# Kernel optimization log

Hardware: AMD Instinct MI355X
Metric: run time of the kernel (lower is better)

The kernel has to match this reference:

```python
import jax, jax.numpy as jnp
import numpy as np

B, C, H, W = 2, 224, 56, 56
NUM_HEADS, HEAD_DIM = 7, 32  # C == NUM_HEADS * HEAD_DIM
EPS = 1e-5


def setup_inputs() -> dict:
    key = jax.random.key(0)
    ks = jax.random.split(key, 16)
    n = lambda k, shape, s=0.05: jax.random.normal(k, shape, dtype=jnp.float32) * s
    return {
        "D": n(ks[0], (B, C, H, W), 1.0),
        "wq": n(ks[1], (2 * C, C)), "bq": n(ks[2], (2 * C,)),
        "wk": n(ks[3], (2 * C, C)), "bk": n(ks[4], (2 * C,)),
        "wv": n(ks[5], (C, C)), "bv": n(ks[6], (C,)),
        "gn_w": jnp.ones((C,), jnp.float32), "gn_b": jnp.zeros((C,), jnp.float32),
        "lambda_init": jnp.array(0.4, jnp.float32),
        "lq1": n(ks[7], (HEAD_DIM,), 0.1), "lk1": n(ks[8], (HEAD_DIM,), 0.1),
        "lq2": n(ks[9], (HEAD_DIM,), 0.1), "lk2": n(ks[10], (HEAD_DIM,), 0.1),
        "w3": n(ks[11], (C, C, 3, 3), 0.02), "b3": n(ks[12], (C,)),
        "wo": n(ks[13], (1, C)), "bo": n(ks[14], (1,)),
    }


def _conv1x1(x, w, b):
    # 1x1 conv == channel-mixing matmul: w [O,C], x [B,C,H,W] -> [B,O,H,W]
    return jnp.einsum('oc,bchw->bohw', w, x) + b[None, :, None, None]


def reference(D, wq, bq, wk, bk, wv, bv, gn_w, gn_b, lambda_init,
              lq1, lk1, lq2, lk2, w3, b3, wo, bo):
    b, c, h_, w_ = D.shape
    N = h_ * w_
    scaling = HEAD_DIM ** (-0.5)

    # spatial coordinate gating: pool over W and over H, broadcast-sum
    x_h = D.mean(axis=3, keepdims=True)          # [B,C,H,1]
    x_w = D.mean(axis=2, keepdims=True)          # [B,C,1,W]
    gated = D * jax.nn.sigmoid(x_h + x_w)

    # GroupNorm with num_groups == C  => per-channel instance norm (biased var)
    mu = gated.mean(axis=(2, 3), keepdims=True)
    var = gated.var(axis=(2, 3), keepdims=True)
    spatial_enh = (gated - mu) / jnp.sqrt(var + EPS)
    spatial_enh = spatial_enh * gn_w[None, :, None, None] + gn_b[None, :, None, None]

    Q = _conv1x1(spatial_enh, wq, bq).reshape(b, 2, NUM_HEADS, HEAD_DIM, N)
    K = _conv1x1(D, wk, bk).reshape(b, 2, NUM_HEADS, HEAD_DIM, N)
    V = _conv1x1(D, wv, bv).reshape(b, NUM_HEADS, HEAD_DIM, N)

    attn1 = jnp.einsum('bhdn,bhdm->bhnm', Q[:, 0], K[:, 0]) * scaling
    attn2 = jnp.einsum('bhdn,bhdm->bhnm', Q[:, 1], K[:, 1]) * scaling

    lam1 = jnp.exp(jnp.sum(lq1 * lk1))
    lam2 = jnp.exp(jnp.sum(lq2 * lk2))
    lam = jnp.clip(lam1 - lam2, 0.0, 1.0) + lambda_init

    attn_weights = jax.nn.softmax(attn1 - lam * attn2, axis=-1)
    out = jnp.einsum('bhnm,bhdm->bhdn', attn_weights, V).reshape(b, c, h_, w_)

    x1 = jax.nn.sigmoid(out.mean(axis=(2, 3), keepdims=True))  # [B,C,1,1]
    x2 = jax.lax.conv_general_dilated(
        out, w3, window_strides=(1, 1), padding='SAME',
        dimension_numbers=('NCHW', 'OIHW', 'NCHW')) + b3[None, :, None, None]
    cross_enh = x2 * x1
    attn_map = jax.nn.sigmoid(_conv1x1(cross_enh, wo, bo))  # [B,1,H,W]
    return attn_map
```

## Files before the change

### kernel.cpp

```cpp
#include <hip/hip_runtime.h>
#include <math.h>

#define NPIX 3136
#define CCH  224
#define SCALING 0.17677669529663687f
#define LOG2E 1.4426950408889634f
#define SCL2 (SCALING * LOG2E)

typedef _Float16 half8_t __attribute__((ext_vector_type(8)));
typedef _Float16 half4_t __attribute__((ext_vector_type(4)));
typedef _Float16 half2_t __attribute__((ext_vector_type(2)));
typedef float floatx4 __attribute__((ext_vector_type(4)));

__device__ __forceinline__ float exp2fast(float x) { return __builtin_amdgcn_exp2f(x); }

__device__ __forceinline__ void blockReduce2(float& a, float& b, float* scratch) {
  #pragma unroll
  for (int off = 32; off > 0; off >>= 1) {
    a += __shfl_down(a, off);
    b += __shfl_down(b, off);
  }
  int wid = threadIdx.x >> 6, lane = threadIdx.x & 63;
  if (lane == 0) { scratch[wid * 2] = a; scratch[wid * 2 + 1] = b; }
  __syncthreads();
  if (threadIdx.x == 0) {
    float sa = 0.f, sb = 0.f;
    #pragma unroll
    for (int i = 0; i < 4; ++i) { sa += scratch[2 * i]; sb += scratch[2 * i + 1]; }
    scratch[0] = sa; scratch[1] = sb;
  }
  __syncthreads();
  a = scratch[0]; b = scratch[1];
}

__global__ void lam_kernel(const float* __restrict__ lq1, const float* __restrict__ lk1,
                           const float* __restrict__ lq2, const float* __restrict__ lk2,
                           const float* __restrict__ lambda_init, float* __restrict__ lam) {
  int t = threadIdx.x;
  float p1 = (t < 32) ? lq1[t] * lk1[t] : 0.f;
  float p2 = (t < 32) ? lq2[t] * lk2[t] : 0.f;
  #pragma unroll
  for (int off = 16; off > 0; off >>= 1) {
    p1 += __shfl_down(p1, off);
    p2 += __shfl_down(p2, off);
  }
  if (t == 0) {
    float d = expf(p1) - expf(p2);
    d = fminf(fmaxf(d, 0.f), 1.f);
    lam[0] = d + lambda_init[0];
  }
}

__global__ __launch_bounds__(256) void prep_kernel(const float* __restrict__ D,
                                                   const float* __restrict__ gn_w,
                                                   const float* __restrict__ gn_b,
                                                   _Float16* __restrict__ senh_h,
                                                   _Float16* __restrict__ Dh) {
  __shared__ float img[NPIX];
  __shared__ float xh[56];
  __shared__ float xw[56];
  __shared__ float scratch[8];
  int bc = blockIdx.x;
  int c = bc % CCH;
  const float* src = D + (size_t)bc * NPIX;
  float4* img4 = (float4*)img;
  const float4* src4 = (const float4*)src;
  half4_t* dh4 = (half4_t*)(Dh + (size_t)bc * NPIX);
  for (int i = threadIdx.x; i < NPIX / 4; i += 256) {
    float4 v = src4[i];
    img4[i] = v;
    half4_t hv;
    hv[0] = (_Float16)v.x; hv[1] = (_Float16)v.y;
    hv[2] = (_Float16)v.z; hv[3] = (_Float16)v.w;
    dh4[i] = hv;
  }
  __syncthreads();
  if (threadIdx.x < 56) {
    int h = threadIdx.x;
    float s = 0.f;
    #pragma unroll 8
    for (int w = 0; w < 56; ++w) s += img[h * 56 + w];
    xh[h] = s * (1.f / 56.f);
  } else if (threadIdx.x >= 64 && threadIdx.x < 120) {
    int w = threadIdx.x - 64;
    float s = 0.f;
    #pragma unroll 8
    for (int h = 0; h < 56; ++h) s += img[h * 56 + w];
    xw[w] = s * (1.f / 56.f);
  }
  __syncthreads();
  float sum = 0.f, ssq = 0.f;
  for (int i = threadIdx.x; i < NPIX; i += 256) {
    int y = i / 56, x = i - y * 56;
    float d = img[i];
    float t = xh[y] + xw[x];
    float sg = 1.f / (1.f + __expf(-t));
    float g = d * sg;
    img[i] = g;
    sum += g;
    ssq += g * g;
  }
  blockReduce2(sum, ssq, scratch);
  float mu = sum * (1.f / (float)NPIX);
  float var = ssq * (1.f / (float)NPIX) - mu * mu;
  float rstd = rsqrtf(var + 1e-5f);
  float a = gn_w[c] * rstd;
  float bb = gn_b[c] - mu * a;
  _Float16* dst = senh_h + (size_t)bc * NPIX;
  for (int i = threadIdx.x; i < NPIX; i += 256) dst[i] = (_Float16)fmaf(img[i], a, bb);
}

__global__ void wcvt_kernel(const float* __restrict__ wq, const float* __restrict__ wk,
                            const float* __restrict__ wv,
                            _Float16* __restrict__ whq, _Float16* __restrict__ whk,
                            _Float16* __restrict__ whv) {
  int i = blockIdx.x * 256 + threadIdx.x;
  const int NQ = 448 * 224 / 4;
  const int NV = 224 * 224 / 4;
  const float* src; _Float16* dst; int off;
  if (i < NQ) { src = wq; dst = whq; off = i; }
  else if (i < 2 * NQ) { src = wk; dst = whk; off = i - NQ; }
  else if (i < 2 * NQ + NV) { src = wv; dst = whv; off = i - 2 * NQ; }
  else return;
  float4 v = ((const float4*)src)[off];
  half4_t h;
  h[0] = (_Float16)v.x; h[1] = (_Float16)v.y;
  h[2] = (_Float16)v.z; h[3] = (_Float16)v.w;
  ((half4_t*)dst)[off] = h;
}

__global__ __launch_bounds__(256) void gemm_f16_kernel(const _Float16* __restrict__ Wh,
                                                       const _Float16* __restrict__ Xh,
                                                       const float* __restrict__ bias,
                                                       _Float16* __restrict__ Y, int M, int mode,
                                                       const float* __restrict__ lamp) {
  __shared__ _Float16 Xs[64][40];
  __shared__ _Float16 Cs[64][72];
  int b = blockIdx.z;
  int r0 = blockIdx.y * 64, n0 = blockIdx.x * 64;
  const _Float16* Xb = Xh + (size_t)b * CCH * NPIX;
  int tid = threadIdx.x;
  int w = tid >> 6, lane = tid & 63, q = lane & 15, g = lane >> 4;

  int wrow = r0 + w * 16 + q;
  if (wrow >= M) wrow = M - 1;
  half8_t wfrag[7];
  #pragma unroll
  for (int kc = 0; kc < 7; ++kc)
    wfrag[kc] = *(const half8_t*)&Wh[(size_t)wrow * 224 + kc * 32 + g * 8];

  floatx4 acc[4];
  #pragma unroll
  for (int t = 0; t < 4; ++t)
    #pragma unroll
    for (int r = 0; r < 4; ++r) acc[t][r] = 0.f;

  int cp = tid & 15, ng = tid >> 4;
  #pragma unroll
  for (int kc = 0; kc < 7; ++kc) {
    const _Float16* x0 = Xb + (size_t)(kc * 32 + 2 * cp) * NPIX + n0 + ng * 4;
    half4_t xa = *(const half4_t*)x0;
    half4_t xb = *(const half4_t*)(x0 + NPIX);
    if (kc) __syncthreads();
    #pragma unroll
    for (int j = 0; j < 4; ++j) {
      half2_t hw; hw[0] = xa[j]; hw[1] = xb[j];
      *(half2_t*)&Xs[ng * 4 + j][2 * cp] = hw;
    }
    __syncthreads();
    #pragma unroll
    for (int t = 0; t < 4; ++t) {
      half8_t xfrag = *(const half8_t*)&Xs[16 * t + q][g * 8];
      acc[t] = __builtin_amdgcn_mfma_f32_16x16x32_f16(wfrag[kc], xfrag, acc[t], 0, 0, 0);
    }
  }

  float lamv = (mode == 1) ? lamp[0] : 0.f;
  #pragma unroll
  for (int t = 0; t < 4; ++t) {
    #pragma unroll
    for (int r = 0; r < 4; ++r) {
      int m = w * 16 + 4 * g + r;
      int n = 16 * t + q;
      int gm = r0 + m;
      float v = 0.f;
      if (gm < M) {
        v = acc[t][r] + bias[gm];
        if (mode == 1) v *= (gm < CCH) ? SCL2 : (-lamv * SCL2);
      }
      Cs[m][n] = (_Float16)v;
    }
  }
  __syncthreads();

  if (mode == 0) {
    int row = tid >> 2, oct = tid & 3;
    if (r0 + row < M) {
      half8_t u0 = *(half8_t*)&Cs[row][oct * 16];
      half8_t u1 = *(half8_t*)&Cs[row][oct * 16 + 8];
      _Float16* dst = Y + ((size_t)b * M + r0 + row) * NPIX + n0 + oct * 16;
      *(half8_t*)dst = u0;
      *(half8_t*)(dst + 8) = u1;
    }
  } else {
    int n = tid & 63, quarter = tid >> 6;
    int vbase = r0 + quarter * 16;
    int chunk = vbase >= CCH;
    int ch_in = vbase - chunk * CCH;
    int hh = ch_in >> 5;
    int dstart = chunk * 32 + (ch_in & 31);
    _Float16 tmp[16];
    #pragma unroll
    for (int i = 0; i < 16; ++i) tmp[i] = Cs[quarter * 16 + i][n];
    _Float16* dst = Y + (((size_t)b * 7 + hh) * NPIX + (n0 + n)) * 64 + dstart;
    *(half8_t*)dst = *(half8_t*)&tmp[0];
    *(half8_t*)(dst + 8) = *(half8_t*)&tmp[8];
  }
}

__global__ __launch_bounds__(256) void attn_part_kernel(const _Float16* __restrict__ Qt,
                                                        const _Float16* __restrict__ Kt,
                                                        const _Float16* __restrict__ Vt,
                                                        float* __restrict__ Opart,
                                                        float2* __restrict__ ml2) {
  __shared__ _Float16 K_lds[2][64][72];
  __shared__ _Float16 V_lds[2][32][72];
  __shared__ _Float16 P_lds[64][72];

  int orig = blockIdx.x;
  int xcd = orig & 7, off = orig >> 3;
  int wg = (xcd < 4) ? xcd * 172 + off : 4 * 172 + (xcd - 4) * 171 + off;
  int qt = wg % 49;
  int rest = wg / 49;
  int seg = rest & 1, bh = rest >> 1;
  int h = bh % 7, b = bh / 7;
  int t0 = seg ? 25 : 0;
  int nt = seg ? 24 : 25;

  int tid = threadIdx.x;
  int w = tid >> 6, lane = tid & 63;
  int q = lane & 15, g = lane >> 4;
  int nq = qt * 64 + w * 16 + q;

  const _Float16* Qb = Qt + ((size_t)(b * 7 + h) * NPIX + nq) * 64;
  const _Float16* Kb = Kt + (size_t)(b * 7 + h) * NPIX * 64;
  const _Float16* Vb = Vt + ((size_t)b * CCH + h * 32) * NPIX;

  half8_t qv[2];
  qv[0] = *(const half8_t*)(Qb + g * 8);
  qv[1] = *(const half8_t*)(Qb + 32 + g * 8);

  floatx4 oacc[2];
  #pragma unroll
  for (int dt = 0; dt < 2; ++dt)
    #pragma unroll
    for (int r = 0; r < 4; ++r) oacc[dt][r] = 0.f;
  float mrun = -INFINITY, lrun = 0.f;

  int kkey = tid >> 2, koct = (tid & 3) * 16;
  const _Float16* ksrc = Kb + ((size_t)t0 * 64 + kkey) * 64 + koct;
  int vd = tid >> 3, voff = (tid & 7) * 8;
  const _Float16* vsrc = Vb + (size_t)vd * NPIX + t0 * 64 + voff;

  half8_t kr0, kr1, vr;
  kr0 = *(const half8_t*)(ksrc);
  kr1 = *(const half8_t*)(ksrc + 8);
  vr = *(const half8_t*)(vsrc);
  *(half8_t*)&K_lds[0][kkey][koct] = kr0;
  *(half8_t*)&K_lds[0][kkey][koct + 8] = kr1;
  *(half8_t*)&V_lds[0][vd][voff] = vr;
  __syncthreads();

  for (int kc = 0; kc < nt; ++kc) {
    int cur = kc & 1;
    if (kc < nt - 1) {
      size_t m0 = (size_t)(kc + 1) * 64;
      kr0 = *(const half8_t*)(ksrc + m0 * 64);
      kr1 = *(const half8_t*)(ksrc + m0 * 64 + 8);
      vr = *(const half8_t*)(vsrc + m0);
    }

    floatx4 sacc[4];
    #pragma unroll
    for (int t = 0; t < 4; ++t)
      #pragma unroll
      for (int r = 0; r < 4; ++r) sacc[t][r] = 0.f;
    #pragma unroll
    for (int t = 0; t < 4; ++t) {
      #pragma unroll
      for (int c = 0; c < 2; ++c) {
        half8_t ka = *(const half8_t*)&K_lds[cur][t * 16 + q][c * 32 + g * 8];
        sacc[t] = __builtin_amdgcn_mfma_f32_16x16x32_f16(ka, qv[c], sacc[t], 0, 0, 0);
      }
    }

    float tmax = fmaxf(fmaxf(sacc[0][0], sacc[0][1]), fmaxf(sacc[0][2], sacc[0][3]));
    #pragma unroll
    for (int t = 1; t < 4; ++t)
      tmax = fmaxf(tmax, fmaxf(fmaxf(sacc[t][0], sacc[t][1]), fmaxf(sacc[t][2], sacc[t][3])));
    tmax = fmaxf(tmax, __shfl_xor(tmax, 16));
    tmax = fmaxf(tmax, __shfl_xor(tmax, 32));
    if (__any(tmax > mrun + 8.f)) {
      float mnew = fmaxf(mrun, tmax);
      float corr = exp2fast(mrun - mnew);
      lrun *= corr;
      #pragma unroll
      for (int dt = 0; dt < 2; ++dt)
        #pragma unroll
        for (int r = 0; r < 4; ++r) oacc[dt][r] *= corr;
      mrun = mnew;
    }
    float lsum = 0.f;
    #pragma unroll
    for (int t = 0; t < 4; ++t)
      #pragma unroll
      for (int r = 0; r < 4; ++r) {
        float p = exp2fast(sacc[t][r] - mrun);
        sacc[t][r] = p;
        lsum += p;
      }
    lsum += __shfl_xor(lsum, 16);
    lsum += __shfl_xor(lsum, 32);
    lrun += lsum;

    #pragma unroll
    for (int t = 0; t < 4; ++t) {
      half4_t ph;
      ph[0] = (_Float16)sacc[t][0];
      ph[1] = (_Float16)sacc[t][1];
      ph[2] = (_Float16)sacc[t][2];
      ph[3] = (_Float16)sacc[t][3];
      *(half4_t*)&P_lds[w * 16 + q][t * 16 + g * 4] = ph;
    }

    #pragma unroll
    for (int dt = 0; dt < 2; ++dt) {
      #pragma unroll
      for (int c = 0; c < 2; ++c) {
        half8_t va = *(const half8_t*)&V_lds[cur][dt * 16 + q][c * 32 + g * 8];
        half8_t pb = *(const half8_t*)&P_lds[w * 16 + q][c * 32 + g * 8];
        oacc[dt] = __builtin_amdgcn_mfma_f32_16x16x32_f16(va, pb, oacc[dt], 0, 0, 0);
      }
    }

    if (kc < nt - 1) {
      *(half8_t*)&K_lds[cur ^ 1][kkey][koct] = kr0;
      *(half8_t*)&K_lds[cur ^ 1][kkey][koct + 8] = kr1;
      *(half8_t*)&V_lds[cur ^ 1][vd][voff] = vr;
    }
    __syncthreads();
  }

  size_t pbase = (((size_t)bh * 2 + seg) * 49 + qt);
  float* out_lds = (float*)&K_lds[0][0][0];
  #pragma unroll
  for (int dt = 0; dt < 2; ++dt)
    #pragma unroll
    for (int r = 0; r < 4; ++r) {
      int d = dt * 16 + g * 4 + r;
      out_lds[d * 68 + w * 16 + q] = oacc[dt][r];
    }
  if (lane < 16) ml2[pbase * 64 + w * 16 + lane] = make_float2(mrun, lrun);
  __syncthreads();
  {
    int d = tid >> 3;
    int i8 = (tid & 7) << 3;
    float4 u0 = *(float4*)&out_lds[d * 68 + i8];
    float4 u1 = *(float4*)&out_lds[d * 68 + i8 + 4];
    float* dst = Opart + pbase * 2048 + d * 64 + i8;
    *(float4*)dst = u0;
    *(float4*)(dst + 4) = u1;
  }
}

__global__ __launch_bounds__(256) void merge_kernel(const float* __restrict__ Opart,
                                                    const float2* __restrict__ ml2,
                                                    float* __restrict__ attno) {
  int blk = blockIdx.x;
  int qt = blk % 49, bh = blk / 49;
  int b = bh / 7, h = bh % 7;
  int tid = threadIdx.x, q = tid & 63, dg = tid >> 6;
  size_t p0 = ((size_t)bh * 2 + 0) * 49 + qt;
  size_t p1 = ((size_t)bh * 2 + 1) * 49 + qt;
  float2 a = ml2[p0 * 64 + q];
  float2 c = ml2[p1 * 64 + q];
  float m = fmaxf(a.x, c.x);
  float w0 = exp2fast(a.x - m), w1 = exp2fast(c.x - m);
  float inv = 1.f / (a.y * w0 + c.y * w1);
  #pragma unroll
  for (int i = 0; i < 8; ++i) {
    int d = dg * 8 + i;
    float o = (Opart[p0 * 2048 + d * 64 + q] * w0 + Opart[p1 * 2048 + d * 64 + q] * w1) * inv;
    attno[((size_t)b * CCH + h * 32 + d) * NPIX + qt * 64 + q] = o;
  }
}

__global__ __launch_bounds__(256) void wx_kernel(const float* __restrict__ out,
                                                 const float* __restrict__ wo,
                                                 const float* __restrict__ b3,
                                                 float* __restrict__ wx,
                                                 float* __restrict__ beff) {
  __shared__ float scratch[8];
  int bc = blockIdx.x;
  int c = bc % CCH;
  int b = bc / CCH;
  const float* src = out + (size_t)bc * NPIX;
  float s = 0.f, dummy = 0.f;
  for (int i = threadIdx.x; i < NPIX; i += 256) s += src[i];
  blockReduce2(s, dummy, scratch);
  if (threadIdx.x == 0) {
    float mean = s * (1.f / (float)NPIX);
    float x1 = 1.f / (1.f + expf(-mean));
    float v = wo[c] * x1;
    wx[bc] = v;
    atomicAdd(&beff[b], v * b3[c]);
  }
}

__global__ void weff_kernel(const float* __restrict__ wx, const float* __restrict__ w3,
                            float* __restrict__ weff) {
  int t = blockIdx.x * 256 + threadIdx.x;
  if (t < 2 * 2016) {
    int b = t / 2016, rem = t - b * 2016;
    const float* wxb = wx + b * CCH;
    float a0 = 0.f, a1 = 0.f, a2 = 0.f, a3 = 0.f;
    for (int c = 0; c < CCH; c += 4) {
      a0 = fmaf(wxb[c + 0], w3[(size_t)(c + 0) * 2016 + rem], a0);
      a1 = fmaf(wxb[c + 1], w3[(size_t)(c + 1) * 2016 + rem], a1);
      a2 = fmaf(wxb[c + 2], w3[(size_t)(c + 2) * 2016 + rem], a2);
      a3 = fmaf(wxb[c + 3], w3[(size_t)(c + 3) * 2016 + rem], a3);
    }
    weff[t] = (a0 + a1) + (a2 + a3);
  }
}

__global__ __launch_bounds__(256) void mk_kernel(const float* __restrict__ attno,
                                                 const float* __restrict__ weff,
                                                 float* __restrict__ Mout) {
  __shared__ float wsh[2016];
  __shared__ float msh[4][9][64];
  int b = blockIdx.y, tile = blockIdx.x;
  int tid = threadIdx.x;
  for (int i = tid; i < 2016; i += 256) wsh[i] = weff[b * 2016 + i];
  __syncthreads();
  int p = tid & 63, s = tid >> 6;
  int px = tile * 64 + p;
  const float* A = attno + (size_t)b * CCH * NPIX + px;
  float m[9];
  #pragma unroll
  for (int k = 0; k < 9; ++k) m[k] = 0.f;
  for (int c = s * 56; c < s * 56 + 56; ++c) {
    float a = A[(size_t)c * NPIX];
    const float* wp = &wsh[c * 9];
    #pragma unroll
    for (int k = 0; k < 9; ++k) m[k] = fmaf(a, wp[k], m[k]);
  }
  #pragma unroll
  for (int k = 0; k < 9; ++k) msh[s][k][p] = m[k];
  __syncthreads();
  for (int i = tid; i < 576; i += 256) {
    int k = i >> 6, p2 = i & 63;
    float v = msh[0][k][p2] + msh[1][k][p2] + msh[2][k][p2] + msh[3][k][p2];
    Mout[((size_t)b * 9 + k) * NPIX + tile * 64 + p2] = v;
  }
}

__global__ void final_kernel(const float* __restrict__ Mout, const float* __restrict__ beff,
                             const float* __restrict__ bo, float* __restrict__ dout) {
  int px = blockIdx.x * 256 + threadIdx.x;
  int b = blockIdx.y;
  if (px >= NPIX) return;
  int y = px / 56, x = px - y * 56;
  const float* Mb = Mout + (size_t)b * 9 * NPIX;
  float s = 0.f;
  #pragma unroll
  for (int ky = 0; ky < 3; ++ky) {
    int yy = y + ky - 1;
    if (yy < 0 || yy >= 56) continue;
    #pragma unroll
    for (int kx = 0; kx < 3; ++kx) {
      int xx = x + kx - 1;
      if (xx < 0 || xx >= 56) continue;
      s += Mb[(ky * 3 + kx) * NPIX + yy * 56 + xx];
    }
  }
  float v = s + beff[b] + bo[0];
  dout[b * NPIX + px] = 1.f / (1.f + expf(-v));
}

extern "C" void kernel_launch(void* const* d_in, const int* in_sizes, int n_in,
                              void* d_out, int out_size, void* d_ws, size_t ws_size,
                              hipStream_t stream) {
  (void)in_sizes; (void)n_in; (void)out_size; (void)ws_size;
  const float* D = (const float*)d_in[0];
  const float* wq = (const float*)d_in[1];
  const float* bq = (const float*)d_in[2];
  const float* wk = (const float*)d_in[3];
  const float* bk = (const float*)d_in[4];
  const float* wv = (const float*)d_in[5];
  const float* bv = (const float*)d_in[6];
  const float* gn_w = (const float*)d_in[7];
  const float* gn_b = (const float*)d_in[8];
  const float* lambda_init = (const float*)d_in[9];
  const float* lq1 = (const float*)d_in[10];
  const float* lk1 = (const float*)d_in[11];
  const float* lq2 = (const float*)d_in[12];
  const float* lk2 = (const float*)d_in[13];
  const float* w3 = (const float*)d_in[14];
  const float* b3 = (const float*)d_in[15];
  const float* wo = (const float*)d_in[16];
  const float* bo = (const float*)d_in[17];

  char* p = (char*)d_ws;
  _Float16* Dh = (_Float16*)p;          p += 2809856;
  _Float16* senh_h = (_Float16*)p;      p += 2809856;
  _Float16* Whq = (_Float16*)p;         p += 200704;
  _Float16* Whk = (_Float16*)p;         p += 200704;
  _Float16* Whv = (_Float16*)p;         p += 100352;
  _Float16* Qt = (_Float16*)p;          p += 5619712;
  _Float16* Kt = (_Float16*)p;          p += 5619712;
  _Float16* Vt = (_Float16*)p;          p += 2809856;
  float* Opart = (float*)p;             p += 11239424;
  float2* ml2 = (float2*)p;             p += 702464;
  float* attno = (float*)p;             p += 5619712;
  float* Mout = (float*)p;              p += 225792;
  float* wx = (float*)p;                p += 1792;
  float* weff = (float*)p;              p += 16128;
  float* beff = (float*)p;              p += 64;
  float* lam = (float*)p;               p += 64;

  hipMemsetAsync(beff, 0, 2 * sizeof(float), stream);
  lam_kernel<<<1, 64, 0, stream>>>(lq1, lk1, lq2, lk2, lambda_init, lam);
  prep_kernel<<<448, 256, 0, stream>>>(D, gn_w, gn_b, senh_h, Dh);
  wcvt_kernel<<<245, 256, 0, stream>>>(wq, wk, wv, Whq, Whk, Whv);
  gemm_f16_kernel<<<dim3(49, 7, 2), 256, 0, stream>>>(Whq, senh_h, bq, Qt, 448, 1, lam);
  gemm_f16_kernel<<<dim3(49, 7, 2), 256, 0, stream>>>(Whk, Dh, bk, Kt, 448, 2, nullptr);
  gemm_f16_kernel<<<dim3(49, 4, 2), 256, 0, stream>>>(Whv, Dh, bv, Vt, 224, 0, nullptr);
  attn_part_kernel<<<1372, 256, 0, stream>>>(Qt, Kt, Vt, Opart, ml2);
  merge_kernel<<<686, 256, 0, stream>>>(Opart, ml2, attno);
  wx_kernel<<<448, 256, 0, stream>>>(attno, wo, b3, wx, beff);
  weff_kernel<<<16, 256, 0, stream>>>(wx, w3, weff);
  mk_kernel<<<dim3(49, 2), 256, 0, stream>>>(attno, weff, Mout);
  final_kernel<<<dim3(13, 2), 256, 0, stream>>>(Mout, beff, bo, (float*)d_out);
}
```

Baseline: 238.7 us.

## Fuse QKV GEMMs, split attention KV into four segments, fold channel means into merge

The three 1x1-conv GEMMs are merged into a single launch, and their input staging is double-buffered so the next K-chunk load overlaps the MFMAs. The attention split-KV now uses four segments instead of two with a simpler XCD remap, and the partial outputs are stored in fp16 to halve that traffic. The merge kernel accumulates per-channel sums through atomics, which removes the separate wx reduction pass, and weff now also computes beff. The prep kernel spreads its row and column pooling over more threads. Trade-offs are fp16 rounding of the partial outputs, more merge work per pixel, and atomic contention.

After: 232.1 us. 2.8% less time.

```diff
diff --git a/kernel.cpp b/kernel.cpp
--- a/kernel.cpp
+++ b/kernel.cpp
@@ -59,6 +59,8 @@
   __shared__ float img[NPIX];
   __shared__ float xh[56];
   __shared__ float xw[56];
+  __shared__ float rp[56][4];
+  __shared__ float cp_[56][4];
   __shared__ float scratch[8];
   int bc = blockIdx.x;
   int c = bc % CCH;
@@ -75,26 +77,35 @@
     dh4[i] = hv;
   }
   __syncthreads();
-  if (threadIdx.x < 56) {
-    int h = threadIdx.x;
+  int t = threadIdx.x;
+  if (t < 224) {
+    int r = t >> 2, qq = t & 3;
     float s = 0.f;
-    #pragma unroll 8
-    for (int w = 0; w < 56; ++w) s += img[h * 56 + w];
-    xh[h] = s * (1.f / 56.f);
-  } else if (threadIdx.x >= 64 && threadIdx.x < 120) {
-    int w = threadIdx.x - 64;
+    #pragma unroll 14
+    for (int j = 0; j < 14; ++j) s += img[r * 56 + qq * 14 + j];
+    rp[r][qq] = s;
+  }
+  __syncthreads();
+  if (t < 224) {
+    int cc = t >> 2, qq = t & 3;
     float s = 0.f;
-    #pragma unroll 8
-    for (int h = 0; h < 56; ++h) s += img[h * 56 + w];
-    xw[w] = s * (1.f / 56.f);
+    #pragma unroll 14
+    for (int j = 0; j < 14; ++j) s += img[(qq * 14 + j) * 56 + cc];
+    cp_[cc][qq] = s;
+  }
+  __syncthreads();
+  if (t < 56) xh[t] = (rp[t][0] + rp[t][1] + rp[t][2] + rp[t][3]) * (1.f / 56.f);
+  else if (t >= 64 && t < 120) {
+    int cc = t - 64;
+    xw[cc] = (cp_[cc][0] + cp_[cc][1] + cp_[cc][2] + cp_[cc][3]) * (1.f / 56.f);
   }
   __syncthreads();
   float sum = 0.f, ssq = 0.f;
   for (int i = threadIdx.x; i < NPIX; i += 256) {
     int y = i / 56, x = i - y * 56;
     float d = img[i];
-    float t = xh[y] + xw[x];
-    float sg = 1.f / (1.f + __expf(-t));
+    float tt = xh[y] + xw[x];
+    float sg = 1.f / (1.f + __expf(-tt));
     float g = d * sg;
     img[i] = g;
     sum += g;
@@ -129,16 +140,32 @@
   ((half4_t*)dst)[off] = h;
 }
 
-__global__ __launch_bounds__(256) void gemm_f16_kernel(const _Float16* __restrict__ Wh,
-                                                       const _Float16* __restrict__ Xh,
-                                                       const float* __restrict__ bias,
-                                                       _Float16* __restrict__ Y, int M, int mode,
+__global__ __launch_bounds__(256) void gemm_qkv_kernel(const _Float16* __restrict__ Whq,
+                                                       const _Float16* __restrict__ Whk,
+                                                       const _Float16* __restrict__ Whv,
+                                                       const _Float16* __restrict__ senh_h,
+                                                       const _Float16* __restrict__ Dh,
+                                                       const float* __restrict__ bq,
+                                                       const float* __restrict__ bk,
+                                                       const float* __restrict__ bv,
+                                                       _Float16* __restrict__ Qt,
+                                                       _Float16* __restrict__ Kt,
+                                                       _Float16* __restrict__ Vt,
                                                        const float* __restrict__ lamp) {
-  __shared__ _Float16 Xs[64][40];
+  __shared__ _Float16 Xs[2][64][40];
   __shared__ _Float16 Cs[64][72];
   int b = blockIdx.z;
-  int r0 = blockIdx.y * 64, n0 = blockIdx.x * 64;
-  const _Float16* Xb = Xh + (size_t)b * CCH * NPIX;
+  int sel = blockIdx.y;
+  int mode, r0, M;
+  const _Float16* Wh;
+  const _Float16* Xb;
+  const float* bias;
+  _Float16* Y;
+  if (sel < 7)       { mode = 1; r0 = sel * 64;        M = 448; Wh = Whq; Xb = senh_h; bias = bq; Y = Qt; }
+  else if (sel < 14) { mode = 2; r0 = (sel - 7) * 64;  M = 448; Wh = Whk; Xb = Dh;     bias = bk; Y = Kt; }
+  else               { mode = 0; r0 = (sel - 14) * 64; M = 224; Wh = Whv; Xb = Dh;     bias = bv; Y = Vt; }
+  Xb += (size_t)b * CCH * NPIX;
+  int n0 = blockIdx.x * 64;
   int tid = threadIdx.x;
   int w = tid >> 6, lane = tid & 63, q = lane & 15, g = lane >> 4;
 
@@ -156,23 +183,39 @@
     for (int r = 0; r < 4; ++r) acc[t][r] = 0.f;
 
   int cp = tid & 15, ng = tid >> 4;
-  #pragma unroll
-  for (int kc = 0; kc < 7; ++kc) {
-    const _Float16* x0 = Xb + (size_t)(kc * 32 + 2 * cp) * NPIX + n0 + ng * 4;
+  {
+    const _Float16* x0 = Xb + (size_t)(2 * cp) * NPIX + n0 + ng * 4;
     half4_t xa = *(const half4_t*)x0;
     half4_t xb = *(const half4_t*)(x0 + NPIX);
-    if (kc) __syncthreads();
     #pragma unroll
     for (int j = 0; j < 4; ++j) {
       half2_t hw; hw[0] = xa[j]; hw[1] = xb[j];
-      *(half2_t*)&Xs[ng * 4 + j][2 * cp] = hw;
+      *(half2_t*)&Xs[0][ng * 4 + j][2 * cp] = hw;
+    }
+  }
+  __syncthreads();
+  #pragma unroll
+  for (int kc = 0; kc < 7; ++kc) {
+    int cur = kc & 1;
+    half4_t xa, xb;
+    if (kc < 6) {
+      const _Float16* x0 = Xb + (size_t)((kc + 1) * 32 + 2 * cp) * NPIX + n0 + ng * 4;
+      xa = *(const half4_t*)x0;
+      xb = *(const half4_t*)(x0 + NPIX);
+    }
+    #pragma unroll
+    for (int t = 0; t < 4; ++t) {
+      half8_t xfrag = *(const half8_t*)&Xs[cur][16 * t + q][g * 8];
+      acc[t] = __builtin_amdgcn_mfma_f32_16x16x32_f16(wfrag[kc], xfrag, acc[t], 0, 0, 0);
+    }
+    if (kc < 6) {
+      #pragma unroll
+      for (int j = 0; j < 4; ++j) {
+        half2_t hw; hw[0] = xa[j]; hw[1] = xb[j];
+        *(half2_t*)&Xs[cur ^ 1][ng * 4 + j][2 * cp] = hw;
+      }
     }
     __syncthreads();
-    #pragma unroll
-    for (int t = 0; t < 4; ++t) {
-      half8_t xfrag = *(const half8_t*)&Xs[16 * t + q][g * 8];
-      acc[t] = __builtin_amdgcn_mfma_f32_16x16x32_f16(wfrag[kc], xfrag, acc[t], 0, 0, 0);
-    }
   }
 
   float lamv = (mode == 1) ? lamp[0] : 0.f;
@@ -198,7 +241,7 @@
     if (r0 + row < M) {
       half8_t u0 = *(half8_t*)&Cs[row][oct * 16];
       half8_t u1 = *(half8_t*)&Cs[row][oct * 16 + 8];
-      _Float16* dst = Y + ((size_t)b * M + r0 + row) * NPIX + n0 + oct * 16;
+      _Float16* dst = Y + ((size_t)b * CCH + r0 + row) * NPIX + n0 + oct * 16;
       *(half8_t*)dst = u0;
       *(half8_t*)(dst + 8) = u1;
     }
@@ -221,21 +264,20 @@
 __global__ __launch_bounds__(256) void attn_part_kernel(const _Float16* __restrict__ Qt,
                                                         const _Float16* __restrict__ Kt,
                                                         const _Float16* __restrict__ Vt,
-                                                        float* __restrict__ Opart,
+                                                        _Float16* __restrict__ Opart,
                                                         float2* __restrict__ ml2) {
   __shared__ _Float16 K_lds[2][64][72];
   __shared__ _Float16 V_lds[2][32][72];
   __shared__ _Float16 P_lds[64][72];
 
   int orig = blockIdx.x;
-  int xcd = orig & 7, off = orig >> 3;
-  int wg = (xcd < 4) ? xcd * 172 + off : 4 * 172 + (xcd - 4) * 171 + off;
+  int wg = (orig & 7) * 343 + (orig >> 3);
   int qt = wg % 49;
   int rest = wg / 49;
-  int seg = rest & 1, bh = rest >> 1;
+  int seg = rest & 3, bh = rest >> 2;
   int h = bh % 7, b = bh / 7;
-  int t0 = seg ? 25 : 0;
-  int nt = seg ? 24 : 25;
+  int t0 = (seg == 0) ? 0 : (12 * seg + 1);
+  int nt = seg ? 12 : 13;
 
   int tid = threadIdx.x;
   int w = tid >> 6, lane = tid & 63;
@@ -351,7 +393,7 @@
     __syncthreads();
   }
 
-  size_t pbase = (((size_t)bh * 2 + seg) * 49 + qt);
+  size_t pbase = (((size_t)bh * 4 + seg) * 49 + qt);
   float* out_lds = (float*)&K_lds[0][0][0];
   #pragma unroll
   for (int dt = 0; dt < 2; ++dt)
@@ -365,72 +407,85 @@
   {
     int d = tid >> 3;
     int i8 = (tid & 7) << 3;
-    float4 u0 = *(float4*)&out_lds[d * 68 + i8];
-    float4 u1 = *(float4*)&out_lds[d * 68 + i8 + 4];
-    float* dst = Opart + pbase * 2048 + d * 64 + i8;
-    *(float4*)dst = u0;
-    *(float4*)(dst + 4) = u1;
-  }
-}
-
-__global__ __launch_bounds__(256) void merge_kernel(const float* __restrict__ Opart,
+    half8_t hv;
+    #pragma unroll
+    for (int j = 0; j < 8; ++j) hv[j] = (_Float16)out_lds[d * 68 + i8 + j];
+    *(half8_t*)(Opart + pbase * 2048 + d * 64 + i8) = hv;
+  }
+}
+
+__global__ __launch_bounds__(256) void merge_kernel(const _Float16* __restrict__ Opart,
                                                     const float2* __restrict__ ml2,
-                                                    float* __restrict__ attno) {
+                                                    float* __restrict__ attno,
+                                                    float* __restrict__ wx_raw) {
   int blk = blockIdx.x;
   int qt = blk % 49, bh = blk / 49;
   int b = bh / 7, h = bh % 7;
   int tid = threadIdx.x, q = tid & 63, dg = tid >> 6;
-  size_t p0 = ((size_t)bh * 2 + 0) * 49 + qt;
-  size_t p1 = ((size_t)bh * 2 + 1) * 49 + qt;
-  float2 a = ml2[p0 * 64 + q];
-  float2 c = ml2[p1 * 64 + q];
-  float m = fmaxf(a.x, c.x);
-  float w0 = exp2fast(a.x - m), w1 = exp2fast(c.x - m);
-  float inv = 1.f / (a.y * w0 + c.y * w1);
+  size_t p0 = (size_t)bh * 4 * 49 + qt;
+  float2 s0 = ml2[(p0 + 0 * 49) * 64 + q];
+  float2 s1 = ml2[(p0 + 1 * 49) * 64 + q];
+  float2 s2 = ml2[(p0 + 2 * 49) * 64 + q];
+  float2 s3 = ml2[(p0 + 3 * 49) * 64 + q];
+  float m = fmaxf(fmaxf(s0.x, s1.x), fmaxf(s2.x, s3.x));
+  float w0 = exp2fast(s0.x - m), w1 = exp2fast(s1.x - m);
+  float w2 = exp2fast(s2.x - m), w3 = exp2fast(s3.x - m);
+  float inv = 1.f / (s0.y * w0 + s1.y * w1 + s2.y * w2 + s3.y * w3);
+  float osum[8];
   #pragma unroll
   for (int i = 0; i < 8; ++i) {
     int d = dg * 8 + i;
-    float o = (Opart[p0 * 2048 + d * 64 + q] * w0 + Opart[p1 * 2048 + d * 64 + q] * w1) * inv;
+    float o = ((float)Opart[(p0 + 0 * 49) * 2048 + d * 64 + q] * w0 +
+               (float)Opart[(p0 + 1 * 49) * 2048 + d * 64 + q] * w1 +
+               (float)Opart[(p0 + 2 * 49) * 2048 + d * 64 + q] * w2 +
+               (float)Opart[(p0 + 3 * 49) * 2048 + d * 64 + q] * w3) * inv;
     attno[((size_t)b * CCH + h * 32 + d) * NPIX + qt * 64 + q] = o;
-  }
-}
-
-__global__ __launch_bounds__(256) void wx_kernel(const float* __restrict__ out,
-                                                 const float* __restrict__ wo,
-                                                 const float* __restrict__ b3,
-                                                 float* __restrict__ wx,
-                                                 float* __restrict__ beff) {
+    osum[i] = o;
+  }
+  #pragma unroll
+  for (int i = 0; i < 8; ++i) {
+    #pragma unroll
+    for (int off = 32; off > 0; off >>= 1) osum[i] += __shfl_xor(osum[i], off);
+  }
+  if ((tid & 63) == 0) {
+    #pragma unroll
+    for (int i = 0; i < 8; ++i)
+      atomicAdd(&wx_raw[b * CCH + h * 32 + dg * 8 + i], osum[i]);
+  }
+}
+
+__global__ __launch_bounds__(256) void weff_kernel(const float* __restrict__ wx_raw,
+                                                   const float* __restrict__ wo,
+                                                   const float* __restrict__ w3,
+                                                   const float* __restrict__ b3,
+                                                   const float* __restrict__ bo,
+                                                   float* __restrict__ weff,
+                                                   float* __restrict__ beff) {
+  __shared__ float wsh[CCH];
   __shared__ float scratch[8];
-  int bc = blockIdx.x;
-  int c = bc % CCH;
-  int b = bc / CCH;
-  const float* src = out + (size_t)bc * NPIX;
-  float s = 0.f, dummy = 0.f;
-  for (int i = threadIdx.x; i < NPIX; i += 256) s += src[i];
-  blockReduce2(s, dummy, scratch);
-  if (threadIdx.x == 0) {
-    float mean = s * (1.f / (float)NPIX);
-    float x1 = 1.f / (1.f + expf(-mean));
-    float v = wo[c] * x1;
-    wx[bc] = v;
-    atomicAdd(&beff[b], v * b3[c]);
-  }
-}
-
-__global__ void weff_kernel(const float* __restrict__ wx, const float* __restrict__ w3,
-                            float* __restrict__ weff) {
-  int t = blockIdx.x * 256 + threadIdx.x;
-  if (t < 2 * 2016) {
-    int b = t / 2016, rem = t - b * 2016;
-    const float* wxb = wx + b * CCH;
+  int b = blockIdx.y;
+  int t = threadIdx.x;
+  if (t < CCH) {
+    float mean = wx_raw[b * CCH + t] * (1.f / (float)NPIX);
+    wsh[t] = wo[t] / (1.f + expf(-mean));
+  }
+  __syncthreads();
+  int rem = blockIdx.x * 252 + t;
+  if (t < 252 && rem < 2016) {
     float a0 = 0.f, a1 = 0.f, a2 = 0.f, a3 = 0.f;
     for (int c = 0; c < CCH; c += 4) {
-      a0 = fmaf(wxb[c + 0], w3[(size_t)(c + 0) * 2016 + rem], a0);
-      a1 = fmaf(wxb[c + 1], w3[(size_t)(c + 1) * 2016 + rem], a1);
-      a2 = fmaf(wxb[c + 2], w3[(size_t)(c + 2) * 2016 + rem], a2);
-      a3 = fmaf(wxb[c + 3], w3[(size_t)(c + 3) * 2016 + rem], a3);
-    }
-    weff[t] = (a0 + a1) + (a2 + a3);
+      a0 = fmaf(wsh[c + 0], w3[(size_t)(c + 0) * 2016 + rem], a0);
+      a1 = fmaf(wsh[c + 1], w3[(size_t)(c + 1) * 2016 + rem], a1);
+      a2 = fmaf(wsh[c + 2], w3[(size_t)(c + 2) * 2016 + rem], a2);
+      a3 = fmaf(wsh[c + 3], w3[(size_t)(c + 3) * 2016 + rem], a3);
+    }
+    weff[b * 2016 + rem] = (a0 + a1) + (a2 + a3);
+  }
+  if (blockIdx.x == 0) {
+    float p = (t < CCH) ? wsh[t] * b3[t] : 0.f;
+    float dummy = 0.f;
+    blockReduce2(p, dummy, scratch);
+    if (t == 0) beff[b] = p + bo[0];
   }
 }
 
@@ -466,7 +521,7 @@
 }
 
 __global__ void final_kernel(const float* __restrict__ Mout, const float* __restrict__ beff,
-                             const float* __restrict__ bo, float* __restrict__ dout) {
+                             float* __restrict__ dout) {
   int px = blockIdx.x * 256 + threadIdx.x;
   int b = blockIdx.y;
   if (px >= NPIX) return;
@@ -484,7 +539,7 @@
       s += Mb[(ky * 3 + kx) * NPIX + yy * 56 + xx];
     }
   }
-  float v = s + beff[b] + bo[0];
+  float v = s + beff[b];
   dout[b * NPIX + px] = 1.f / (1.f + expf(-v));
 }
 
@@ -520,26 +575,24 @@
   _Float16* Qt = (_Float16*)p;          p += 5619712;
   _Float16* Kt = (_Float16*)p;          p += 5619712;
   _Float16* Vt = (_Float16*)p;          p += 2809856;
-  float* Opart = (float*)p;             p += 11239424;
-  float2* ml2 = (float2*)p;             p += 702464;
+  _Float16* Opart = (_Float16*)p;       p += 11239424;
+  float2* ml2 = (float2*)p;             p += 1404928;
   float* attno = (float*)p;             p += 5619712;
   float* Mout = (float*)p;              p += 225792;
-  float* wx = (float*)p;                p += 1792;
-  float* weff = (float*)p;              p += 16128;
+  float* wx_raw = (float*)p;            p += 1792;
   float* beff = (float*)p;              p += 64;
   float* lam = (float*)p;               p += 64;
-
-  hipMemsetAsync(beff, 0, 2 * sizeof(float), stream);
+  float* weff = (float*)p;              p += 16128;
+
+  hipMemsetAsync(wx_raw, 0, 1792 + 64, stream);
   lam_kernel<<<1, 64, 0, stream>>>(lq1, lk1, lq2, lk2, lambda_init, lam);
   prep_kernel<<<448, 256, 0, stream>>>(D, gn_w, gn_b, senh_h, Dh);
   wcvt_kernel<<<245, 256, 0, stream>>>(wq, wk, wv, Whq, Whk, Whv);
-  gemm_f16_kernel<<<dim3(49, 7, 2), 256, 0, stream>>>(Whq, senh_h, bq, Qt, 448, 1, lam);
-  gemm_f16_kernel<<<dim3(49, 7, 2), 256, 0, stream>>>(Whk, Dh, bk, Kt, 448, 2, nullptr);
-  gemm_f16_kernel<<<dim3(49, 4, 2), 256, 0, stream>>>(Whv, Dh, bv, Vt, 224, 0, nullptr);
-  attn_part_kernel<<<1372, 256, 0, stream>>>(Qt, Kt, Vt, Opart, ml2);
-  merge_kernel<<<686, 256, 0, stream>>>(Opart, ml2, attno);
-  wx_kernel<<<448, 256, 0, stream>>>(attno, wo, b3, wx, beff);
-  weff_kernel<<<16, 256, 0, stream>>>(wx, w3, weff);
+  gemm_qkv_kernel<<<dim3(49, 18, 2), 256, 0, stream>>>(Whq, Whk, Whv, senh_h, Dh,
+                                                       bq, bk, bv, Qt, Kt, Vt, lam);
+  attn_part_kernel<<<2744, 256, 0, stream>>>(Qt, Kt, Vt, Opart, ml2);
+  merge_kernel<<<686, 256, 0, stream>>>(Opart, ml2, attno, wx_raw);
+  weff_kernel<<<dim3(8, 2), 256, 0, stream>>>(wx_raw, wo, w3, b3, bo, weff, beff);
   mk_kernel<<<dim3(49, 2), 256, 0, stream>>>(attno, weff, Mout);
-  final_kernel<<<dim3(13, 2), 256, 0, stream>>>(Mout, beff, bo, (float*)d_out);
-}
+  final_kernel<<<dim3(13, 2), 256, 0, stream>>>(Mout, beff, (float*)d_out);
+}
```
